# Kernel optimization log

Hardware: AMD Instinct MI355X
Metric: run time of the kernel (lower is better)

## Reference

```python
import jax, jax.numpy as jnp
import numpy as np

N, E, DIN, DH, DOUT, NB = 50000, 400000, 32, 128, 16, 2

def setup_inputs() -> dict:
    key = jax.random.key(0)
    ks = jax.random.split(key, 16)
    s = 0.05
    inp = {
        "inputs": jax.random.normal(ks[0], (N, DIN), jnp.float32),
        "frames": jax.random.normal(ks[1], (N, 3, 3), jnp.float32),
        "edge_index": jax.random.randint(ks[2], (2, E), 0, N, jnp.int32),
        # GraphNet in/out projections
        "win": jax.random.normal(ks[3], (DIN, DH), jnp.float32) * s,
        "bin_": jnp.zeros((DH,), jnp.float32),
        "wout": jax.random.normal(ks[4], (DH, DOUT), jnp.float32) * s,
        "bout": jnp.zeros((DOUT,), jnp.float32),
        # per-block EdgeConv params, stacked over NB blocks
        # mlp1: Linear(2*DH, DH) -> ReLU -> Linear(DH, DH) -> ReLU -> Linear(DH, DH)
        "w1a": jax.random.normal(ks[5], (NB, 2 * DH, DH), jnp.float32) * s,
        "b1a": jnp.zeros((NB, DH), jnp.float32),
        "w1b": jax.random.normal(ks[6], (NB, DH, DH), jnp.float32) * s,
        "b1b": jnp.zeros((NB, DH), jnp.float32),
        "w1c": jax.random.normal(ks[7], (NB, DH, DH), jnp.float32) * s,
        "b1c": jnp.zeros((NB, DH), jnp.float32),
        # mlp2: Linear(DH, DH) -> ReLU -> Linear(DH, DH)
        "w2a": jax.random.normal(ks[8], (NB, DH, DH), jnp.float32) * s,
        "b2a": jnp.zeros((NB, DH), jnp.float32),
        "w2b": jax.random.normal(ks[9], (NB, DH, DH), jnp.float32) * s,
        "b2b": jnp.zeros((NB, DH), jnp.float32),
    }
    return inp


def reference(inputs, frames, edge_index, win, bin_, wout, bout,
              w1a, b1a, w1b, b1b, w1c, b1c, w2a, b2a, w2b, b2b):
    src = edge_index[0]  # j: message source
    dst = edge_index[1]  # i: aggregation target (PyG convention)
    x = inputs @ win + bin_  # [N, DH]
    for b in range(NB):
        x_j = x[src]  # [E, DH] gather
        x_i = x[dst]  # [E, DH] gather
        m = jnp.concatenate([x_j, x_i], axis=-1)  # [E, 2*DH]
        m = jax.nn.relu(m @ w1a[b] + b1a[b])
        m = jax.nn.relu(m @ w1b[b] + b1b[b])
        m = m @ w1c[b] + b1c[b]  # [E, DH]
        agg = jax.ops.segment_sum(m, dst, num_segments=N)  # aggr='add'
        h = jax.nn.relu(agg @ w2a[b] + b2a[b])
        x = h @ w2b[b] + b2b[b]
    return x @ wout + bout  # [N, DOUT]
```

## Files before the change

### kernel.cpp

```cpp
#include <hip/hip_runtime.h>

#define NN 50000
#define NE 400000
#define DIN 32
#define DH  128
#define DOUT 16
#define NB  2
#define NBLK 49

typedef _Float16 half8 __attribute__((ext_vector_type(8)));
typedef _Float16 half4 __attribute__((ext_vector_type(4)));
typedef float    f32x4 __attribute__((ext_vector_type(4)));

#define FENCE() asm volatile("s_waitcnt lgkmcnt(0)" ::: "memory")
#define MFMA16(a, b, c) __builtin_amdgcn_mfma_f32_16x16x32_f16((a), (b), (c), 0, 0, 0)

__global__ void k_node_proj(const float* __restrict__ inp,
                            const float* __restrict__ win,
                            const float* __restrict__ bin,
                            _Float16* __restrict__ x16) {
    int gid = blockIdx.x * blockDim.x + threadIdx.x;
    if (gid >= NN * DH) return;
    int n = gid >> 7, h = gid & 127;
    float acc = bin[h];
    const float* row = inp + (size_t)n * DIN;
#pragma unroll
    for (int k = 0; k < DIN; ++k) acc = fmaf(row[k], win[k * DH + h], acc);
    x16[gid] = (_Float16)acc;
}

__global__ void k_wprep(const float* __restrict__ w1a, const float* __restrict__ w1b,
                        const float* __restrict__ w1c, const float* __restrict__ w2a,
                        const float* __restrict__ w2b, _Float16* __restrict__ wf) {
    int c = blockIdx.x * blockDim.x + threadIdx.x;
    if (c >= NB * 12288) return;
    int b = c / 12288, r = c % 12288;
    int tt = r >> 9, rem = r & 511;
    const float* W; int t;
    if (tt < 8)       { W = w1a + (size_t)b * 2 * DH * DH; t = tt; }
    else if (tt < 12) { W = w1b + (size_t)b * DH * DH; t = tt - 8; }
    else if (tt < 16) { W = w1c + (size_t)b * DH * DH; t = tt - 12; }
    else if (tt < 20) { W = w2a + (size_t)b * DH * DH; t = tt - 16; }
    else              { W = w2b + (size_t)b * DH * DH; t = tt - 20; }
    int n = rem >> 6, l = rem & 63;
    int row0 = t * 32 + (l >> 4) * 8, col = n * 16 + (l & 15);
    half8 v;
#pragma unroll
    for (int j = 0; j < 8; ++j) v[j] = (_Float16)W[(size_t)(row0 + j) * DH + col];
    *(half8*)(wf + (size_t)c * 8) = v;
}

__global__ void k_woutprep(const float* __restrict__ wout, _Float16* __restrict__ wf) {
    int c = threadIdx.x;
    int t = c >> 6, l = c & 63;
    half8 v;
#pragma unroll
    for (int j = 0; j < 8; ++j)
        v[j] = (_Float16)wout[(size_t)(t * 32 + (l >> 4) * 8 + j) * DOUT + (l & 15)];
    *(half8*)(wf + (size_t)c * 8) = v;
}

__global__ void k_hist(const int* __restrict__ dstI, int* __restrict__ deg) {
    int e = blockIdx.x * blockDim.x + threadIdx.x;
    if (e < NE) atomicAdd(&deg[dstI[e]], 1);
}

__global__ void __launch_bounds__(1024) k_scanA(const int* __restrict__ deg,
                                                int* __restrict__ bsum) {
    __shared__ int ws[16];
    int tid = threadIdx.x, wv = tid >> 6, l = tid & 63;
    int i = blockIdx.x * 1024 + tid;
    int v = (i < NN) ? deg[i] : 0;
#pragma unroll
    for (int off = 32; off; off >>= 1) v += __shfl_down(v, off);
    if (l == 0) ws[wv] = v;
    __syncthreads();
    if (tid == 0) {
        int s = 0;
#pragma unroll
        for (int k = 0; k < 16; ++k) s += ws[k];
        bsum[blockIdx.x] = s;
    }
}

__global__ void k_scanB(const int* __restrict__ bsum, int* __restrict__ boff) {
    int l = threadIdx.x;
    int v = (l < NBLK) ? bsum[l] : 0;
    int s = v;
#pragma unroll
    for (int off = 1; off < 64; off <<= 1) {
        int t = __shfl_up(s, off);
        if (l >= off) s += t;
    }
    if (l < NBLK) boff[l] = s - v;
}

__global__ void __launch_bounds__(1024) k_scanC(const int* __restrict__ deg,
                                                const int* __restrict__ boff,
                                                int* __restrict__ cur) {
    __shared__ int ws[16];
    int tid = threadIdx.x, wv = tid >> 6, l = tid & 63;
    int i = blockIdx.x * 1024 + tid;
    int v = (i < NN) ? deg[i] : 0;
    int s = v;
#pragma unroll
    for (int off = 1; off < 64; off <<= 1) {
        int t = __shfl_up(s, off);
        if (l >= off) s += t;
    }
    if (l == 63) ws[wv] = s;
    __syncthreads();
    if (wv == 0) {
        int t = (l < 16) ? ws[l] : 0;
#pragma unroll
        for (int off = 1; off < 16; off <<= 1) {
            int u = __shfl_up(t, off);
            if (l >= off) t += u;
        }
        if (l < 16) ws[l] = t;
    }
    __syncthreads();
    int base = boff[blockIdx.x] + (wv ? ws[wv - 1] : 0);
    if (i < NN) cur[i] = base + s - v;
}

__global__ void k_scatter(const int* __restrict__ srcI, const int* __restrict__ dstI,
                          int* __restrict__ cur, int* __restrict__ eS,
                          int* __restrict__ eD) {
    int e = blockIdx.x * blockDim.x + threadIdx.x;
    if (e >= NE) return;
    int d = dstI[e];
    int p = atomicAdd(&cur[d], 1);
    eS[p] = srcI[e];
    eD[p] = d;
}

__global__ void __launch_bounds__(256, 5) k_edge5(
    const _Float16* __restrict__ xin,
    const int* __restrict__ eS, const int* __restrict__ eD,
    const half8* __restrict__ wfa, const half8* __restrict__ wfb,
    const half8* __restrict__ wfc,
    const float* __restrict__ b1a, const float* __restrict__ b1b,
    const float* __restrict__ b1c,
    float* __restrict__ agg) {
    __shared__ _Float16 sm[8192];
    __shared__ int slotT[4][64];

    const int tid = threadIdx.x, wv = tid >> 6, l = tid & 63;
    const int lm = l & 15, lk = l >> 4;
    const int nb = wv * 2;
    const int ebase = blockIdx.x * 64;

    int srcs[4], dsts[4];
#pragma unroll
    for (int s = 0; s < 4; ++s) {
        srcs[s] = eS[ebase + s * 16 + lm];
        dsts[s] = eD[ebase + s * 16 + lm];
    }

    int dl = eD[ebase + l];
    int prev = __shfl(dl, (l == 0) ? 0 : l - 1);
    bool bit = ((l & 31) == 0) ? true : (dl != prev);
    unsigned long long bal = __ballot(bit);
    unsigned mlo = (unsigned)bal, mhi = (unsigned)(bal >> 32);
    unsigned myM = (l < 32) ? mlo : mhi;
    int ll = l & 31;
    int slot_l = __popc(myM << (31 - ll)) - 1;
    if (bit) slotT[wv][(l >> 5) * 32 + slot_l] = dl;
    int nlo = __popc(mlo), nhi = __popc(mhi);

    float ba[2], bb[2], bc[2];
#pragma unroll
    for (int q = 0; q < 2; ++q) {
        ba[q] = b1a[(nb + q) * 16 + lm];
        bb[q] = b1b[(nb + q) * 16 + lm];
        bc[q] = b1c[(nb + q) * 16 + lm];
    }

    const f32x4 z = {0.f, 0.f, 0.f, 0.f};
    f32x4 acc[4][2];
    half8 aC[4], aN[4], wC[2], wN[2];

#pragma unroll
    for (int s = 0; s < 4; ++s)
#pragma unroll
        for (int q = 0; q < 2; ++q) acc[s][q] = z;
#pragma unroll
    for (int s = 0; s < 4; ++s)
        aC[s] = *(const half8*)(xin + (size_t)srcs[s] * DH + lk * 8);
#pragma unroll
    for (int q = 0; q < 2; ++q) wC[q] = wfa[(size_t)(nb + q) * 64 + l];

    for (int t = 0; t < 8; ++t) {
        if (t < 7) {
            int t1 = t + 1;
#pragma unroll
            for (int s = 0; s < 4; ++s) {
                int node = (t1 < 4) ? srcs[s] : dsts[s];
                aN[s] = *(const half8*)(xin + (size_t)node * DH + (t1 & 3) * 32 + lk * 8);
            }
#pragma unroll
            for (int q = 0; q < 2; ++q)
                wN[q] = wfa[(size_t)(t1 * 8 + nb + q) * 64 + l];
        }
#pragma unroll
        for (int q = 0; q < 2; ++q)
#pragma unroll
            for (int s = 0; s < 4; ++s)
                acc[s][q] = MFMA16(aC[s], wC[q], acc[s][q]);
#pragma unroll
        for (int s = 0; s < 4; ++s) aC[s] = aN[s];
#pragma unroll
        for (int q = 0; q < 2; ++q) wC[q] = wN[q];
    }
#pragma unroll
    for (int s = 0; s < 4; ++s)
#pragma unroll
        for (int q = 0; q < 2; ++q) {
            int n = nb + q;
            int base = s * 2048 +
                       ((n >> 1) * 64 + ((n & 1) * 2 + (lm >> 3)) * 16 + lk * 4) * 8 +
                       (lm & 7);
#pragma unroll
            for (int j = 0; j < 4; ++j)
                sm[base + j * 8] = (_Float16)fmaxf(acc[s][q][j] + ba[q], 0.f);
        }
    __syncthreads();

#pragma unroll
    for (int s = 0; s < 4; ++s)
#pragma unroll
        for (int q = 0; q < 2; ++q) acc[s][q] = z;
#pragma unroll
    for (int q = 0; q < 2; ++q) wC[q] = wfb[(size_t)(nb + q) * 64 + l];
    for (int t = 0; t < 4; ++t) {
        if (t < 3)
#pragma unroll
            for (int q = 0; q < 2; ++q)
                wN[q] = wfb[(size_t)((t + 1) * 8 + nb + q) * 64 + l];
#pragma unroll
        for (int s = 0; s < 4; ++s)
            aC[s] = *(const half8*)&sm[s * 2048 + (t * 64 + l) * 8];
#pragma unroll
        for (int q = 0; q < 2; ++q)
#pragma unroll
            for (int s = 0; s < 4; ++s)
                acc[s][q] = MFMA16(aC[s], wC[q], acc[s][q]);
#pragma unroll
        for (int q = 0; q < 2; ++q) wC[q] = wN[q];
    }
    __syncthreads();
#pragma unroll
    for (int s = 0; s < 4; ++s)
#pragma unroll
        for (int q = 0; q < 2; ++q) {
            int n = nb + q;
            int base = s * 2048 +
                       ((n >> 1) * 64 + ((n & 1) * 2 + (lm >> 3)) * 16 + lk * 4) * 8 +
                       (lm & 7);
#pragma unroll
            for (int j = 0; j < 4; ++j)
                sm[base + j * 8] = (_Float16)fmaxf(acc[s][q][j] + bb[q], 0.f);
        }
    __syncthreads();

#pragma unroll
    for (int s = 0; s < 4; ++s)
#pragma unroll
        for (int q = 0; q < 2; ++q) acc[s][q] = z;
#pragma unroll
    for (int q = 0; q < 2; ++q) wC[q] = wfc[(size_t)(nb + q) * 64 + l];
    for (int t = 0; t < 4; ++t) {
        if (t < 3)
#pragma unroll
            for (int q = 0; q < 2; ++q)
                wN[q] = wfc[(size_t)((t + 1) * 8 + nb + q) * 64 + l];
#pragma unroll
        for (int s = 0; s < 4; ++s)
            aC[s] = *(const half8*)&sm[s * 2048 + (t * 64 + l) * 8];
#pragma unroll
        for (int q = 0; q < 2; ++q)
#pragma unroll
            for (int s = 0; s < 4; ++s)
                acc[s][q] = MFMA16(aC[s], wC[q], acc[s][q]);
#pragma unroll
        for (int q = 0; q < 2; ++q) wC[q] = wN[q];
    }
    __syncthreads();

#pragma unroll
    for (int s = 0; s < 4; ++s) {
        int h = s >> 1;
        int e0 = (s * 16 + lk * 4) & 31;
#pragma unroll
        for (int q = 0; q < 2; ++q) {
            int n = nb + q;
            half4 v;
#pragma unroll
            for (int j = 0; j < 4; ++j) v[j] = (_Float16)(acc[s][q][j] + bc[q]);
            *(half4*)&sm[h * 4096 + (n * 64 + (e0 >> 3) * 16 + lm) * 8 + (e0 & 7)] = v;
        }
    }
    FENCE();

#pragma unroll
    for (int h = 0; h < 2; ++h) {
        const int nsl = h ? nhi : nlo;
        half8 ind0, ind1;
#pragma unroll
        for (int e8 = 0; e8 < 8; ++e8) {
            int se = __shfl(slot_l, h * 32 + lk * 8 + e8);
            ind0[e8] = (se == lm)      ? (_Float16)1.f : (_Float16)0.f;
            ind1[e8] = (se == lm + 16) ? (_Float16)1.f : (_Float16)0.f;
        }
        int dS[4], dS2[4];
#pragma unroll
        for (int r = 0; r < 4; ++r) {
            int s = lk * 4 + r;
            dS[r]  = (s < nsl && s < 16) ? slotT[wv][h * 32 + s] : -1;
            int s2 = 16 + s;
            dS2[r] = (s2 < nsl) ? slotT[wv][h * 32 + s2] : -1;
        }
#pragma unroll
        for (int q = 0; q < 2; ++q) {
            int g = nb + q;
            half8 bfrag = *(const half8*)&sm[(h * 512 + g * 64 + l) * 8];
            f32x4 p = MFMA16(ind0, bfrag, z);
#pragma unroll
            for (int r = 0; r < 4; ++r)
                if (dS[r] >= 0)
                    unsafeAtomicAdd(agg + (size_t)dS[r] * DH + g * 16 + lm, p[r]);
            if (nsl > 16) {
                f32x4 p2 = MFMA16(ind1, bfrag, z);
#pragma unroll
                for (int r = 0; r < 4; ++r)
                    if (dS2[r] >= 0)
                        unsafeAtomicAdd(agg + (size_t)dS2[r] * DH + g * 16 + lm, p2[r]);
            }
        }
    }
}

template <bool LAST>
__global__ void __launch_bounds__(256, 4) k_node_mfma(
    const float* __restrict__ agg,
    const half8* __restrict__ wfa, const half8* __restrict__ wfb,
    const float* __restrict__ b2a, const float* __restrict__ b2b,
    _Float16* __restrict__ xo,
    const half8* __restrict__ woutf, const float* __restrict__ bout,
    float* __restrict__ out) {
    __shared__ _Float16 sM[4][2048];
    const int tid = threadIdx.x, wv = tid >> 6, l = tid & 63;
    const int lm = l & 15, lk = l >> 4;
    const int n0 = (blockIdx.x * 4 + wv) * 16;
    if (n0 >= NN) return;
    int nodeA = n0 + lm;
    if (nodeA >= NN) nodeA = NN - 1;

    float b2ar[8], b2br[8];
#pragma unroll
    for (int n = 0; n < 8; ++n) {
        b2ar[n] = b2a[n * 16 + lm];
        b2br[n] = b2b[n * 16 + lm];
    }

    const f32x4 z = {0.f, 0.f, 0.f, 0.f};
    f32x4 acc[8];
#pragma unroll
    for (int n = 0; n < 8; ++n) acc[n] = z;

    for (int t = 0; t < 4; ++t) {
        const float* ap = agg + (size_t)nodeA * DH + t * 32 + lk * 8;
        float4 v0 = *(const float4*)ap;
        float4 v1 = *(const float4*)(ap + 4);
        half8 a;
        a[0] = (_Float16)v0.x; a[1] = (_Float16)v0.y;
        a[2] = (_Float16)v0.z; a[3] = (_Float16)v0.w;
        a[4] = (_Float16)v1.x; a[5] = (_Float16)v1.y;
        a[6] = (_Float16)v1.z; a[7] = (_Float16)v1.w;
        const half8* wp = wfa + (size_t)t * 512 + l;
#pragma unroll
        for (int n = 0; n < 8; ++n) acc[n] = MFMA16(a, wp[n * 64], acc[n]);
    }
    _Float16* sm = sM[wv];
#pragma unroll
    for (int n = 0; n < 8; ++n) {
        int base = ((n >> 1) * 64 + ((n & 1) * 2 + (lm >> 3)) * 16 + lk * 4) * 8 +
                   (lm & 7);
#pragma unroll
        for (int j = 0; j < 4; ++j)
            sm[base + j * 8] = (_Float16)fmaxf(acc[n][j] + b2ar[n], 0.f);
    }
    FENCE();
#pragma unroll
    for (int n = 0; n < 8; ++n) acc[n] = z;
    for (int t = 0; t < 4; ++t) {
        half8 a = *(const half8*)&sm[(t * 64 + l) * 8];
        const half8* wp = wfb + (size_t)t * 512 + l;
#pragma unroll
        for (int n = 0; n < 8; ++n) acc[n] = MFMA16(a, wp[n * 64], acc[n]);
    }
    if (!LAST) {
#pragma unroll
        for (int n = 0; n < 8; ++n) {
#pragma unroll
            for (int j = 0; j < 4; ++j) {
                int nd = n0 + lk * 4 + j;
                if (nd < NN)
                    xo[(size_t)nd * DH + n * 16 + lm] = (_Float16)(acc[n][j] + b2br[n]);
            }
        }
    } else {
        FENCE();
#pragma unroll
        for (int n = 0; n < 8; ++n) {
            int base = ((n >> 1) * 64 + ((n & 1) * 2 + (lm >> 3)) * 16 + lk * 4) * 8 +
                       (lm & 7);
#pragma unroll
            for (int j = 0; j < 4; ++j)
                sm[base + j * 8] = (_Float16)(acc[n][j] + b2br[n]);
        }
        FENCE();
        f32x4 ao = z;
        for (int t = 0; t < 4; ++t) {
            half8 a = *(const half8*)&sm[(t * 64 + l) * 8];
            ao = MFMA16(a, woutf[t * 64 + l], ao);
        }
        float bo = bout[lm];
#pragma unroll
        for (int j = 0; j < 4; ++j) {
            int nd = n0 + lk * 4 + j;
            if (nd < NN) out[(size_t)nd * DOUT + lm] = ao[j] + bo;
        }
    }
}

extern "C" void kernel_launch(void* const* d_in, const int* in_sizes, int n_in,
                              void* d_out, int out_size, void* d_ws, size_t ws_size,
                              hipStream_t stream) {
    const float* inputs = (const float*)d_in[0];
    const int* eidx = (const int*)d_in[2];
    const int* srcI = eidx;
    const int* dstI = eidx + NE;
    const float* win  = (const float*)d_in[3];
    const float* bin_ = (const float*)d_in[4];
    const float* wout = (const float*)d_in[5];
    const float* bout = (const float*)d_in[6];
    const float* w1a = (const float*)d_in[7];
    const float* b1a = (const float*)d_in[8];
    const float* w1b = (const float*)d_in[9];
    const float* b1b = (const float*)d_in[10];
    const float* w1c = (const float*)d_in[11];
    const float* b1c = (const float*)d_in[12];
    const float* w2a = (const float*)d_in[13];
    const float* b2a = (const float*)d_in[14];
    const float* w2b = (const float*)d_in[15];
    const float* b2b = (const float*)d_in[16];

    char* p = (char*)d_ws;
    _Float16* xa = (_Float16*)p;    p += (size_t)NN * DH * 2;
    _Float16* xb = (_Float16*)p;    p += (size_t)NN * DH * 2;
    _Float16* wfAll = (_Float16*)p; p += ((size_t)NB * 12288 + 256) * 16;
    float* agg   = (float*)p;       p += (size_t)NN * DH * 4;
    int* deg     = (int*)p;         p += (size_t)NN * 4;
    int* cur     = (int*)p;         p += (size_t)NN * 4;
    int* bsum    = (int*)p;         p += 256;
    int* boff    = (int*)p;         p += 256;
    int* eSrt    = (int*)p;         p += (size_t)NE * 4;
    int* eDrt    = (int*)p;         p += (size_t)NE * 4;
    float* out   = (float*)d_out;
    _Float16* wfW = wfAll + (size_t)NB * 12288 * 8;

    k_wprep<<<(NB * 12288 + 255) / 256, 256, 0, stream>>>(w1a, w1b, w1c, w2a, w2b, wfAll);
    k_woutprep<<<1, 256, 0, stream>>>(wout, wfW);
    k_node_proj<<<(NN * DH + 255) / 256, 256, 0, stream>>>(inputs, win, bin_, xa);

    hipMemsetAsync(deg, 0, (size_t)NN * 4, stream);
    k_hist<<<(NE + 255) / 256, 256, 0, stream>>>(dstI, deg);
    k_scanA<<<NBLK, 1024, 0, stream>>>(deg, bsum);
    k_scanB<<<1, 64, 0, stream>>>(bsum, boff);
    k_scanC<<<NBLK, 1024, 0, stream>>>(deg, boff, cur);
    k_scatter<<<(NE + 255) / 256, 256, 0, stream>>>(srcI, dstI, cur, eSrt, eDrt);

    for (int b = 0; b < NB; ++b) {
        const _Float16* xi = (b & 1) ? xb : xa;
        _Float16*       xo = (b & 1) ? xa : xb;
        hipMemsetAsync(agg, 0, (size_t)NN * DH * 4, stream);
        const half8* whalf = (const half8*)(wfAll + (size_t)b * 12288 * 8);
        k_edge5<<<NE / 64, 256, 0, stream>>>(
            xi, eSrt, eDrt, whalf, whalf + 4096, whalf + 6144,
            b1a + (size_t)b * DH, b1b + (size_t)b * DH, b1c + (size_t)b * DH,
            agg);
        if (b < NB - 1)
            k_node_mfma<false><<<(NN + 63) / 64, 256, 0, stream>>>(
                agg, whalf + 8192, whalf + 10240,
                b2a + (size_t)b * DH, b2b + (size_t)b * DH,
                xo, (const half8*)wfW, bout, out);
        else
            k_node_mfma<true><<<(NN + 63) / 64, 256, 0, stream>>>(
                agg, whalf + 8192, whalf + 10240,
                b2a + (size_t)b * DH, b2b + (size_t)b * DH,
                xo, (const half8*)wfW, bout, out);
    }
}
```

Measured before the change: 370.0 us.

## Swap MFMA operands so edge MLP intermediates stay in-lane with vectorized LDS stores

The edge kernel now computes transposed tiles (weights as the A operand), so each lane holds 4 consecutive output features per edge. Intermediate activations can then be written to shared memory as single half8 vector stores instead of scalar scattered stores. The weights for w1b/w1c are pre-permuted on the host-side prep kernel to match the new K ordering. Bias loads become float4 loads, slotT reads are vectorized, an XOR swizzle is added to the final staging layout to reduce bank conflicts, and the occupancy hint drops from 5 to 4 blocks per CU.

```diff
diff --git a/kernel.cpp b/kernel.cpp
--- a/kernel.cpp
+++ b/kernel.cpp
@@ -9,7 +9,6 @@
 #define NBLK 49
 
 typedef _Float16 half8 __attribute__((ext_vector_type(8)));
-typedef _Float16 half4 __attribute__((ext_vector_type(4)));
 typedef float    f32x4 __attribute__((ext_vector_type(4)));
 
 #define FENCE() asm volatile("s_waitcnt lgkmcnt(0)" ::: "memory")
@@ -42,11 +41,16 @@
     else if (tt < 16) { W = w1c + (size_t)b * DH * DH; t = tt - 12; }
     else if (tt < 20) { W = w2a + (size_t)b * DH * DH; t = tt - 16; }
     else              { W = w2b + (size_t)b * DH * DH; t = tt - 20; }
+    bool perm = (tt >= 8 && tt < 16);
     int n = rem >> 6, l = rem & 63;
-    int row0 = t * 32 + (l >> 4) * 8, col = n * 16 + (l & 15);
+    int col = n * 16 + (l & 15);
     half8 v;
 #pragma unroll
-    for (int j = 0; j < 8; ++j) v[j] = (_Float16)W[(size_t)(row0 + j) * DH + col];
+    for (int j = 0; j < 8; ++j) {
+        int row = perm ? ((2 * t + (j >> 2)) * 16 + (l >> 4) * 4 + (j & 3))
+                       : (t * 32 + (l >> 4) * 8 + j);
+        v[j] = (_Float16)W[(size_t)row * DH + col];
+    }
     *(half8*)(wf + (size_t)c * 8) = v;
 }
 
@@ -135,7 +139,7 @@
     eD[p] = d;
 }
 
-__global__ void __launch_bounds__(256, 5) k_edge5(
+__global__ void __launch_bounds__(256, 4) k_edge8(
     const _Float16* __restrict__ xin,
     const int* __restrict__ eS, const int* __restrict__ eD,
     const half8* __restrict__ wfa, const half8* __restrict__ wfb,
@@ -169,14 +173,6 @@
     if (bit) slotT[wv][(l >> 5) * 32 + slot_l] = dl;
     int nlo = __popc(mlo), nhi = __popc(mhi);
 
-    float ba[2], bb[2], bc[2];
-#pragma unroll
-    for (int q = 0; q < 2; ++q) {
-        ba[q] = b1a[(nb + q) * 16 + lm];
-        bb[q] = b1b[(nb + q) * 16 + lm];
-        bc[q] = b1c[(nb + q) * 16 + lm];
-    }
-
     const f32x4 z = {0.f, 0.f, 0.f, 0.f};
     f32x4 acc[4][2];
     half8 aC[4], aN[4], wC[2], wN[2];
@@ -207,24 +203,26 @@
         for (int q = 0; q < 2; ++q)
 #pragma unroll
             for (int s = 0; s < 4; ++s)
-                acc[s][q] = MFMA16(aC[s], wC[q], acc[s][q]);
+                acc[s][q] = MFMA16(wC[q], aC[s], acc[s][q]);
 #pragma unroll
         for (int s = 0; s < 4; ++s) aC[s] = aN[s];
 #pragma unroll
         for (int q = 0; q < 2; ++q) wC[q] = wN[q];
     }
-#pragma unroll
-    for (int s = 0; s < 4; ++s)
-#pragma unroll
-        for (int q = 0; q < 2; ++q) {
-            int n = nb + q;
-            int base = s * 2048 +
-                       ((n >> 1) * 64 + ((n & 1) * 2 + (lm >> 3)) * 16 + lk * 4) * 8 +
-                       (lm & 7);
-#pragma unroll
-            for (int j = 0; j < 4; ++j)
-                sm[base + j * 8] = (_Float16)fmaxf(acc[s][q][j] + ba[q], 0.f);
-        }
+    {
+        float4 B0 = *(const float4*)(b1a + nb * 16 + lk * 4);
+        float4 B1 = *(const float4*)(b1a + (nb + 1) * 16 + lk * 4);
+#pragma unroll
+        for (int s = 0; s < 4; ++s) {
+            half8 v;
+#pragma unroll
+            for (int j = 0; j < 4; ++j) {
+                v[j]     = (_Float16)fmaxf(acc[s][0][j] + (&B0.x)[j], 0.f);
+                v[4 + j] = (_Float16)fmaxf(acc[s][1][j] + (&B1.x)[j], 0.f);
+            }
+            *(half8*)&sm[((wv * 4 + s) * 64 + l) * 8] = v;
+        }
+    }
     __syncthreads();
 
 #pragma unroll
@@ -240,28 +238,30 @@
                 wN[q] = wfb[(size_t)((t + 1) * 8 + nb + q) * 64 + l];
 #pragma unroll
         for (int s = 0; s < 4; ++s)
-            aC[s] = *(const half8*)&sm[s * 2048 + (t * 64 + l) * 8];
+            aC[s] = *(const half8*)&sm[((t * 4 + s) * 64 + l) * 8];
 #pragma unroll
         for (int q = 0; q < 2; ++q)
 #pragma unroll
             for (int s = 0; s < 4; ++s)
-                acc[s][q] = MFMA16(aC[s], wC[q], acc[s][q]);
+                acc[s][q] = MFMA16(wC[q], aC[s], acc[s][q]);
 #pragma unroll
         for (int q = 0; q < 2; ++q) wC[q] = wN[q];
     }
     __syncthreads();
-#pragma unroll
-    for (int s = 0; s < 4; ++s)
-#pragma unroll
-        for (int q = 0; q < 2; ++q) {
-            int n = nb + q;
-            int base = s * 2048 +
-                       ((n >> 1) * 64 + ((n & 1) * 2 + (lm >> 3)) * 16 + lk * 4) * 8 +
-                       (lm & 7);
-#pragma unroll
-            for (int j = 0; j < 4; ++j)
-                sm[base + j * 8] = (_Float16)fmaxf(acc[s][q][j] + bb[q], 0.f);
-        }
+    {
+        float4 B0 = *(const float4*)(b1b + nb * 16 + lk * 4);
+        float4 B1 = *(const float4*)(b1b + (nb + 1) * 16 + lk * 4);
+#pragma unroll
+        for (int s = 0; s < 4; ++s) {
+            half8 v;
+#pragma unroll
+            for (int j = 0; j < 4; ++j) {
+                v[j]     = (_Float16)fmaxf(acc[s][0][j] + (&B0.x)[j], 0.f);
+                v[4 + j] = (_Float16)fmaxf(acc[s][1][j] + (&B1.x)[j], 0.f);
+            }
+            *(half8*)&sm[((wv * 4 + s) * 64 + l) * 8] = v;
+        }
+    }
     __syncthreads();
 
 #pragma unroll
@@ -277,28 +277,35 @@
                 wN[q] = wfc[(size_t)((t + 1) * 8 + nb + q) * 64 + l];
 #pragma unroll
         for (int s = 0; s < 4; ++s)
-            aC[s] = *(const half8*)&sm[s * 2048 + (t * 64 + l) * 8];
+            aC[s] = *(const half8*)&sm[((t * 4 + s) * 64 + l) * 8];
 #pragma unroll
         for (int q = 0; q < 2; ++q)
 #pragma unroll
             for (int s = 0; s < 4; ++s)
-                acc[s][q] = MFMA16(aC[s], wC[q], acc[s][q]);
+                acc[s][q] = MFMA16(wC[q], aC[s], acc[s][q]);
 #pragma unroll
         for (int q = 0; q < 2; ++q) wC[q] = wN[q];
     }
     __syncthreads();
 
-#pragma unroll
-    for (int s = 0; s < 4; ++s) {
-        int h = s >> 1;
-        int e0 = (s * 16 + lk * 4) & 31;
-#pragma unroll
-        for (int q = 0; q < 2; ++q) {
-            int n = nb + q;
-            half4 v;
-#pragma unroll
-            for (int j = 0; j < 4; ++j) v[j] = (_Float16)(acc[s][q][j] + bc[q]);
-            *(half4*)&sm[h * 4096 + (n * 64 + (e0 >> 3) * 16 + lm) * 8 + (e0 & 7)] = v;
+    {
+        float4 C0 = *(const float4*)(b1c + nb * 16 + lk * 4);
+        float4 C1 = *(const float4*)(b1c + (nb + 1) * 16 + lk * 4);
+#pragma unroll
+        for (int s = 0; s < 4; ++s) {
+            int h = s >> 1;
+            int ldb = (s & 1) * 32 + (lm >> 3) * 16;
+#pragma unroll
+            for (int q = 0; q < 2; ++q) {
+#pragma unroll
+                for (int j = 0; j < 4; ++j) {
+                    int idx = wv * 2048 +
+                              ((h * 2 + q) * 64 + ldb + lk * 4 + j) * 8 + (lm & 7);
+                    idx ^= (lm >> 3) << 4;
+                    float bv = q ? (&C1.x)[j] : (&C0.x)[j];
+                    sm[idx] = (_Float16)(acc[s][q][j] + bv);
+                }
+            }
         }
     }
     FENCE();
@@ -313,18 +320,20 @@
             ind0[e8] = (se == lm)      ? (_Float16)1.f : (_Float16)0.f;
             ind1[e8] = (se == lm + 16) ? (_Float16)1.f : (_Float16)0.f;
         }
+        int4 dv  = *(const int4*)&slotT[wv][h * 32 + lk * 4];
+        int4 dv2 = *(const int4*)&slotT[wv][h * 32 + 16 + lk * 4];
         int dS[4], dS2[4];
 #pragma unroll
         for (int r = 0; r < 4; ++r) {
-            int s = lk * 4 + r;
-            dS[r]  = (s < nsl && s < 16) ? slotT[wv][h * 32 + s] : -1;
-            int s2 = 16 + s;
-            dS2[r] = (s2 < nsl) ? slotT[wv][h * 32 + s2] : -1;
+            int s0 = lk * 4 + r;
+            dS[r]  = (s0 < nsl && s0 < 16) ? (&dv.x)[r] : -1;
+            dS2[r] = (16 + s0 < nsl) ? (&dv2.x)[r] : -1;
         }
 #pragma unroll
         for (int q = 0; q < 2; ++q) {
             int g = nb + q;
-            half8 bfrag = *(const half8*)&sm[(h * 512 + g * 64 + l) * 8];
+            int bidx = (wv * 2048 + ((h * 2 + q) * 64 + l) * 8) ^ (((l >> 4) & 1) << 4);
+            half8 bfrag = *(const half8*)&sm[bidx];
             f32x4 p = MFMA16(ind0, bfrag, z);
 #pragma unroll
             for (int r = 0; r < 4; ++r)
@@ -487,7 +496,7 @@
         _Float16*       xo = (b & 1) ? xa : xb;
         hipMemsetAsync(agg, 0, (size_t)NN * DH * 4, stream);
         const half8* whalf = (const half8*)(wfAll + (size_t)b * 12288 * 8);
-        k_edge5<<<NE / 64, 256, 0, stream>>>(
+        k_edge8<<<NE / 64, 256, 0, stream>>>(
             xi, eSrt, eDrt, whalf, whalf + 4096, whalf + 6144,
             b1a + (size_t)b * DH, b1b + (size_t)b * DH, b1c + (size_t)b * DH,
             agg);
```

Measured after the change: 367.0 us. Within noise of the previous version (-0.8%).
